# Performance work log

Hardware: AMD Instinct MI355X
Metric: run time of the kernel (lower is better)

The kernel has to match this reference:

```python
import jax, jax.numpy as jnp
import numpy as np

B, L, H, P = 4, 8192, 256, 256


def discretize(log_real, imag, log_Delta, B_real, B_imag):
    # Lambda = -exp(log_real) + i*imag ; ZOH discretization
    Lr = -jnp.exp(log_real)
    Li = imag
    Delta = jnp.exp(log_Delta)
    ad = Lr * Delta
    bd = Li * Delta
    exp_ad = jnp.exp(ad)
    Lbar_r = exp_ad * jnp.cos(bd)
    Lbar_i = exp_ad * jnp.sin(bd)
    denom = jnp.maximum(Lr * Lr + Li * Li, 1e-12)
    inv_Lr = Lr / denom
    inv_Li = -Li / denom
    diff_r = Lbar_r - 1.0
    diff_i = Lbar_i
    coeff_r = inv_Lr * diff_r - inv_Li * diff_i
    coeff_i = inv_Lr * diff_i + inv_Li * diff_r
    B_bar_r = coeff_r[:, None] * B_real - coeff_i[:, None] * B_imag
    B_bar_i = coeff_r[:, None] * B_imag + coeff_i[:, None] * B_real
    return Lbar_r, Lbar_i, B_bar_r, B_bar_i


def binop(ei, ej):
    Ar_i, Ai_i, xr_i, xi_i = ei
    Ar_j, Ai_j, xr_j, xi_j = ej
    return (Ar_j * Ar_i - Ai_j * Ai_i,
            Ar_j * Ai_i + Ai_j * Ar_i,
            Ar_j * xr_i - Ai_j * xi_i + xr_j,
            Ar_j * xi_i + Ai_j * xr_i + xi_j)


def apply_ssm(Lbar_r, Lbar_i, B_bar_r, B_bar_i, C_real, C_imag, D, x):
    # x: (B,L,H), B_bar: (P,H), C: (H,P)
    Bu_r = jnp.einsum('blh,ph->blp', x, B_bar_r)
    Bu_i = jnp.einsum('blh,ph->blp', x, B_bar_i)
    A_r = jnp.broadcast_to(Lbar_r, Bu_r.shape)
    A_i = jnp.broadcast_to(Lbar_i, Bu_i.shape)
    _, _, xs_r, xs_i = jax.lax.associative_scan(binop, (A_r, A_i, Bu_r, Bu_i), axis=1)
    ys = jnp.einsum('blp,hp->blh', xs_r, C_real) - jnp.einsum('blp,hp->blh', xs_i, C_imag)
    return ys + D * x


def s5(log_real, imag, log_Delta, B_real, B_imag, C_real, C_imag, D, x):
    Lbar_r, Lbar_i, B_bar_r, B_bar_i = discretize(log_real, imag, log_Delta, B_real, B_imag)
    y = apply_ssm(Lbar_r, Lbar_i, B_bar_r, B_bar_i, C_real, C_imag, D, x)
    return jax.nn.gelu(y, approximate=False)


def setup_inputs() -> dict:
    key = jax.random.key(0)
    ks = jax.random.split(key, 17)
    std_b = 1.0 / H ** 0.5
    std_c = 1.0 / P ** 0.5
    def params(ki):
        k = jax.random.split(ks[ki], 8)
        return dict(
            log_real=jax.random.normal(k[0], (P,), jnp.float32) * 0.5,
            imag=jax.random.normal(k[1], (P,), jnp.float32),
            log_Delta=jnp.zeros((P,), jnp.float32),
            B_real=jax.random.normal(k[2], (P, H), jnp.float32) * std_b,
            B_imag=jax.random.normal(k[3], (P, H), jnp.float32) * std_b,
            C_real=jax.random.normal(k[4], (H, P), jnp.float32) * std_c,
            C_imag=jax.random.normal(k[5], (H, P), jnp.float32) * std_c,
            D=jnp.ones((H,), jnp.float32),
        )
    f = params(1)
    b = params(2)
    inp = {'x': jax.random.normal(ks[0], (B, L, H), jnp.float32)}
    for name, v in f.items():
        inp['fwd_' + name] = v
    for name, v in b.items():
        inp['bwd_' + name] = v
    return inp


def reference(x,
              fwd_log_real, fwd_imag, fwd_log_Delta, fwd_B_real, fwd_B_imag,
              fwd_C_real, fwd_C_imag, fwd_D,
              bwd_log_real, bwd_imag, bwd_log_Delta, bwd_B_real, bwd_B_imag,
              bwd_C_real, bwd_C_imag, bwd_D):
    x_flip = jnp.flip(x, axis=1)
    y_f = s5(fwd_log_real, fwd_imag, fwd_log_Delta, fwd_B_real, fwd_B_imag,
             fwd_C_real, fwd_C_imag, fwd_D, x)
    y_b = s5(bwd_log_real, bwd_imag, bwd_log_Delta, bwd_B_real, bwd_B_imag,
             bwd_C_real, bwd_C_imag, bwd_D, x_flip)
    return y_f + jnp.flip(y_b, axis=1)
```

## Files before the change

### kernel.cpp

```cpp
#include <hip/hip_runtime.h>
#include <math.h>

#define B_DIM 4
#define L_DIM 8192
#define H_DIM 256
#define P_DIM 256
#define M_DIM (B_DIM * L_DIM)
#define NC 64
#define LC 128

typedef __attribute__((ext_vector_type(8))) short bf16x8;
typedef __attribute__((ext_vector_type(4))) float f32x4;

static __device__ __forceinline__ float bf2f(unsigned int u) {
    union { unsigned int i; float f; } v; v.i = u << 16; return v.f;
}
static __device__ __forceinline__ unsigned short f2bf(float f) {
    union { float f; unsigned int i; } v; v.f = f;
    unsigned int r = v.i + 0x7FFFu + ((v.i >> 16) & 1u);
    return (unsigned short)(r >> 16);
}
static __device__ __forceinline__ float gelu_f(float x) {
    float z = 0.7978845608028654f * (x + 0.044715f * x * x * x);
    float e = __expf(2.0f * z);
    float t = 1.0f - 2.0f / (e + 1.0f);
    return 0.5f * x * (1.0f + t);
}
static __device__ __forceinline__ void async_load16(const void* g, void* l) {
    __builtin_amdgcn_global_load_lds(
        (const __attribute__((address_space(1))) unsigned int*)g,
        (__attribute__((address_space(3))) unsigned int*)l, 16, 0, 0);
}

__global__ void prep_kernel(const float* fLr, const float* fIm, const float* fLd,
                            const float* fBr, const float* fBi,
                            const float* fCr, const float* fCi,
                            const float* bLr, const float* bIm, const float* bLd,
                            const float* bBr, const float* bBi,
                            const float* bCr, const float* bCi,
                            const float4* __restrict__ x4, ushort4* __restrict__ xb,
                            unsigned short* Bmat, unsigned short* B3, float2* LbarWS) {
    int gid = blockIdx.x * 256 + threadIdx.x;
    if (gid < 2097152) {
        float4 v = x4[gid];
        ushort4 o;
        o.x = f2bf(v.x); o.y = f2bf(v.y); o.z = f2bf(v.z); o.w = f2bf(v.w);
        xb[gid] = o;
        return;
    }
    int g1 = gid - 2097152;
    if (g1 < 262144) {
        int k = g1 >> 8, h = g1 & 255;
        int d = k >> 9, pc = k & 511, p = pc >> 1, comp = pc & 1;
        const float* LR = d ? bLr : fLr;
        const float* IM = d ? bIm : fIm;
        const float* LD = d ? bLd : fLd;
        const float* BR = d ? bBr : fBr;
        const float* BI = d ? bBi : fBi;
        float Lr = -expf(LR[p]);
        float Li = IM[p];
        float Delta = expf(LD[p]);
        float ea = expf(Lr * Delta);
        float bd = Li * Delta;
        float Lbr = ea * cosf(bd);
        float Lbi = ea * sinf(bd);
        float denom = fmaxf(Lr * Lr + Li * Li, 1e-12f);
        float ivr = Lr / denom, ivi = -Li / denom;
        float dr = Lbr - 1.0f, di = Lbi;
        float cr = ivr * dr - ivi * di;
        float ci = ivr * di + ivi * dr;
        float br = BR[p * 256 + h], bi = BI[p * 256 + h];
        float val = comp ? (cr * bi + ci * br) : (cr * br - ci * bi);
        Bmat[g1] = f2bf(val);
    } else if (g1 < 524288) {
        int g2 = g1 - 262144;
        int d = g2 >> 17;
        int rem = g2 & 131071;
        int h = rem >> 9;
        int kk = rem & 511;
        int p = kk >> 1, comp = kk & 1;
        const float* CR = d ? bCr : fCr;
        const float* CI = d ? bCi : fCi;
        float val = comp ? -CI[h * 256 + p] : CR[h * 256 + p];
        B3[g2] = f2bf(val);
    } else if (g1 < 524800) {
        int g2 = g1 - 524288;
        int d = g2 >> 8, p = g2 & 255;
        const float* LR = d ? bLr : fLr;
        const float* IM = d ? bIm : fIm;
        const float* LD = d ? bLd : fLd;
        float Lr = -expf(LR[p]); float Li = IM[p]; float Delta = expf(LD[p]);
        float ea = expf(Lr * Delta); float bd = Li * Delta;
        LbarWS[g2] = make_float2(ea * cosf(bd), ea * sinf(bd));
    }
}

__global__ __launch_bounds__(256, 2) void k1_gemm(const unsigned short* __restrict__ A,
                                                  const unsigned short* __restrict__ Bm,
                                                  unsigned short* __restrict__ Bu,
                                                  const float2* __restrict__ Lbar,
                                                  float2* __restrict__ carry,
                                                  float2* __restrict__ halfc) {
    __shared__ unsigned short SH[16384];
    __shared__ float2 Sbuf[64];
    int tid = threadIdx.x;
    int lane = tid & 63, wv = tid >> 6;
    int wm = (wv >> 1) * 64, wn = (wv & 1) * 64;
    int Mb = blockIdx.x * 128, Nb = blockIdx.y * 128;
    int lr = lane >> 3;
    int swz = ((lane & 7) ^ lr) * 8;
    f32x4 acc[4][4];
#pragma unroll
    for (int i = 0; i < 4; i++)
#pragma unroll
        for (int j = 0; j < 4; j++) acc[i][j] = (f32x4){0.f, 0.f, 0.f, 0.f};
    int mrow = lane & 15, quad = lane >> 4;
    for (int kb = 0; kb < 256; kb += 64) {
#pragma unroll
        for (int ch = wv; ch < 16; ch += 4) {
            int r = ch * 8 + lr;
            async_load16(A  + (size_t)(Mb + r) * 256 + kb + swz, (char*)SH + ch * 1024);
            async_load16(Bm + (size_t)(Nb + r) * 256 + kb + swz, (char*)SH + 16384 + ch * 1024);
        }
        __syncthreads();
#pragma unroll
        for (int kk = 0; kk < 64; kk += 32) {
            bf16x8 af[4], bfr[4];
#pragma unroll
            for (int i = 0; i < 4; i++) {
                int rr = wm + 16 * i + mrow;
                af[i] = *(const bf16x8*)&SH[rr * 64 + ((((kk >> 3) + quad) ^ (rr & 7)) << 3)];
            }
#pragma unroll
            for (int j = 0; j < 4; j++) {
                int rr = wn + 16 * j + mrow;
                bfr[j] = *(const bf16x8*)&SH[8192 + rr * 64 + ((((kk >> 3) + quad) ^ (rr & 7)) << 3)];
            }
#pragma unroll
            for (int i = 0; i < 4; i++)
#pragma unroll
                for (int j = 0; j < 4; j++)
                    acc[i][j] = __builtin_amdgcn_mfma_f32_16x16x32_bf16(af[i], bfr[j], acc[i][j], 0, 0, 0);
        }
        __syncthreads();
    }
    unsigned short* Cs = SH;
#pragma unroll
    for (int i = 0; i < 4; i++)
#pragma unroll
        for (int j = 0; j < 4; j++)
#pragma unroll
            for (int r = 0; r < 4; r++) {
                int row = wm + 16 * i + quad * 4 + r;
                int col = wn + 16 * j + mrow;
                Cs[row * 128 + col] = f2bf(acc[i][j][r]);
            }
    __syncthreads();
#pragma unroll
    for (int it = 0; it < 8; it++) {
        int o = tid * 16 + it * 4096;
        int row = o >> 8, colb = o & 255;
        uint4 v = *(const uint4*)((const char*)Cs + o);
        *(uint4*)((char*)Bu + (size_t)(Mb + row) * 2048 + (size_t)Nb * 2 + colb) = v;
    }
    int d = Nb >> 9;
    int b = Mb >> 13;
    int c = (Mb >> 7) & 63;
    float sr = 0.f, si = 0.f;
    float2 A2 = make_float2(0.f, 0.f);
    int p = 0;
    if (tid < 128) {
        int j = tid & 63, half = tid >> 6;
        p = ((Nb & 511) >> 1) + j;
        A2 = Lbar[d * 256 + p];
        const unsigned int* C32 = (const unsigned int*)Cs;
        int r0 = half * 64;
        if (d == 0) {
            for (int t = 0; t < 64; t++) {
                unsigned int v = C32[(r0 + t) * 64 + j];
                float zr = bf2f(v & 0xffffu), zi = bf2f(v >> 16);
                float nr = A2.x * sr - A2.y * si + zr;
                float ni = A2.x * si + A2.y * sr + zi;
                sr = nr; si = ni;
            }
        } else {
            for (int t = 63; t >= 0; t--) {
                unsigned int v = C32[(r0 + t) * 64 + j];
                float zr = bf2f(v & 0xffffu), zi = bf2f(v >> 16);
                float nr = A2.x * sr - A2.y * si + zr;
                float ni = A2.x * si + A2.y * sr + zi;
                sr = nr; si = ni;
            }
        }
        if (half == 1) Sbuf[j] = make_float2(sr, si);
    }
    __syncthreads();
    if (tid < 64) {
        float2 S1 = Sbuf[tid];
        float a64r = A2.x, a64i = A2.y;
#pragma unroll
        for (int k = 0; k < 6; k++) {
            float nr = a64r * a64r - a64i * a64i;
            float ni = 2.f * a64r * a64i;
            a64r = nr; a64i = ni;
        }
        float cr, ci;
        float2 hv;
        if (d == 0) {
            cr = a64r * sr - a64i * si + S1.x;
            ci = a64r * si + a64i * sr + S1.y;
            hv = make_float2(sr, si);
        } else {
            cr = sr + a64r * S1.x - a64i * S1.y;
            ci = si + a64r * S1.y + a64i * S1.x;
            hv = S1;
        }
        size_t cidx = ((size_t)(d * 4 + b) * NC + c) * 256 + p;
        carry[cidx] = make_float2(cr, ci);
        halfc[cidx] = hv;
    }
}

__global__ __launch_bounds__(512) void scan_fix_kernel(unsigned int* __restrict__ XSu,
                                                       const float2* __restrict__ Lbar,
                                                       const float2* __restrict__ carry,
                                                       const float2* __restrict__ halfc) {
    int m = blockIdx.x, b = blockIdx.y;
    int c = m >> 1, h = m & 1;
    int d = threadIdx.x >> 8;
    int p = threadIdx.x & 255;
    float2 A = Lbar[d * 256 + p];
    float ar = A.x, ai = A.y;
    float a64r = ar, a64i = ai;
#pragma unroll
    for (int k = 0; k < 6; k++) {
        float nr = a64r * a64r - a64i * a64i;
        float ni = 2.f * a64r * a64i;
        a64r = nr; a64i = ni;
    }
    float a128r = a64r * a64r - a64i * a64i;
    float a128i = 2.f * a64r * a64i;
    float sr = 0.f, si = 0.f;
    const float2* cb = carry + ((size_t)(d * 4 + b) * NC) * 256 + p;
    size_t hidx = ((size_t)(d * 4 + b) * NC + c) * 256 + p;
    if (d == 0) {
#pragma unroll 4
        for (int j = 0; j < c; j++) {
            float2 cj = cb[(size_t)j * 256];
            float nr = a128r * sr - a128i * si + cj.x;
            float ni = a128r * si + a128i * sr + cj.y;
            sr = nr; si = ni;
        }
        if (h) {
            float2 hc = halfc[hidx];
            float nr = a64r * sr - a64i * si + hc.x;
            float ni = a64r * si + a64i * sr + hc.y;
            sr = nr; si = ni;
        }
    } else {
#pragma unroll 4
        for (int j = NC - 1; j > c; j--) {
            float2 cj = cb[(size_t)j * 256];
            float nr = a128r * sr - a128i * si + cj.x;
            float ni = a128r * si + a128i * sr + cj.y;
            sr = nr; si = ni;
        }
        if (!h) {
            float2 hc = halfc[hidx];
            float nr = a64r * sr - a64i * si + hc.x;
            float ni = a64r * si + a64i * sr + hc.y;
            sr = nr; si = ni;
        }
    }
    size_t base = (size_t)b * L_DIM * 512 + d * 256 + p;
    int l0 = c * 128 + h * 64;
    if (d == 0) {
#pragma unroll 16
        for (int t = 0; t < 64; t++) {
            size_t idx = base + (size_t)(l0 + t) * 512;
            unsigned int v = XSu[idx];
            float zr = bf2f(v & 0xffffu), zi = bf2f(v >> 16);
            float nr = ar * sr - ai * si + zr;
            float ni = ar * si + ai * sr + zi;
            sr = nr; si = ni;
            XSu[idx] = (unsigned int)f2bf(sr) | ((unsigned int)f2bf(si) << 16);
        }
    } else {
#pragma unroll 16
        for (int t = 63; t >= 0; t--) {
            size_t idx = base + (size_t)(l0 + t) * 512;
            unsigned int v = XSu[idx];
            float zr = bf2f(v & 0xffffu), zi = bf2f(v >> 16);
            float nr = ar * sr - ai * si + zr;
            float ni = ar * si + ai * sr + zi;
            sr = nr; si = ni;
            XSu[idx] = (unsigned int)f2bf(sr) | ((unsigned int)f2bf(si) << 16);
        }
    }
}

static __device__ __forceinline__ void k3_half(const unsigned short* __restrict__ XS,
                                               const unsigned short* __restrict__ B3h,
                                               unsigned short* As, unsigned short* Bs,
                                               int Mb, int Hb, int coff,
                                               int wm, int wn, int mrow, int quad,
                                               int lr, int swz, int wv,
                                               f32x4 (&acc)[4][4]) {
    for (int kb = 0; kb < 512; kb += 64) {
#pragma unroll
        for (int ch = wv; ch < 16; ch += 4) {
            int r = ch * 8 + lr;
            async_load16(XS + (size_t)(Mb + r) * 1024 + coff + kb + swz, (char*)As + ch * 1024);
            async_load16(B3h + (size_t)(Hb + r) * 512 + kb + swz, (char*)Bs + ch * 1024);
        }
        __syncthreads();
#pragma unroll
        for (int kk = 0; kk < 64; kk += 32) {
            bf16x8 af[4], bfr[4];
#pragma unroll
            for (int i = 0; i < 4; i++) {
                int rr = wm + 16 * i + mrow;
                af[i] = *(const bf16x8*)&As[rr * 64 + ((((kk >> 3) + quad) ^ (rr & 7)) << 3)];
            }
#pragma unroll
            for (int j = 0; j < 4; j++) {
                int rr = wn + 16 * j + mrow;
                bfr[j] = *(const bf16x8*)&Bs[rr * 64 + ((((kk >> 3) + quad) ^ (rr & 7)) << 3)];
            }
#pragma unroll
            for (int i = 0; i < 4; i++)
#pragma unroll
                for (int j = 0; j < 4; j++)
                    acc[i][j] = __builtin_amdgcn_mfma_f32_16x16x32_bf16(af[i], bfr[j], acc[i][j], 0, 0, 0);
        }
        __syncthreads();
    }
}

__global__ __launch_bounds__(256, 2) void k3_gemm(const unsigned short* __restrict__ XS,
                                                  const unsigned short* __restrict__ B3,
                                                  const unsigned short* __restrict__ xbf,
                                                  const float* __restrict__ Df,
                                                  const float* __restrict__ Db,
                                                  float* __restrict__ out) {
    __shared__ unsigned short As[128 * 64];
    __shared__ unsigned short Bs[128 * 64];
    int tid = threadIdx.x;
    int lane = tid & 63, wv = tid >> 6;
    int wm = (wv >> 1) * 64, wn = (wv & 1) * 64;
    int Mb = blockIdx.x * 128, Hb = blockIdx.y * 128;
    int lr = lane >> 3;
    int swz = ((lane & 7) ^ lr) * 8;
    int mrow = lane & 15, quad = lane >> 4;
    f32x4 accf[4][4], accb[4][4];
#pragma unroll
    for (int i = 0; i < 4; i++)
#pragma unroll
        for (int j = 0; j < 4; j++) {
            accf[i][j] = (f32x4){0.f, 0.f, 0.f, 0.f};
            accb[i][j] = (f32x4){0.f, 0.f, 0.f, 0.f};
        }
    k3_half(XS, B3,          As, Bs, Mb, Hb, 0,   wm, wn, mrow, quad, lr, swz, wv, accf);
    k3_half(XS, B3 + 131072, As, Bs, Mb, Hb, 512, wm, wn, mrow, quad, lr, swz, wv, accb);
#pragma unroll
    for (int i = 0; i < 4; i++)
#pragma unroll
        for (int j = 0; j < 4; j++) {
            int h = Hb + wn + 16 * j + mrow;
            float df = Df[h], db = Db[h];
#pragma unroll
            for (int r = 0; r < 4; r++) {
                int row = Mb + wm + 16 * i + quad * 4 + r;
                float xv = bf2f((unsigned int)xbf[(size_t)row * 256 + h]);
                float yf = accf[i][j][r] + df * xv;
                float yb = accb[i][j][r] + db * xv;
                out[(size_t)row * 256 + h] = gelu_f(yf) + gelu_f(yb);
            }
        }
}

extern "C" void kernel_launch(void* const* d_in, const int* in_sizes, int n_in,
                              void* d_out, int out_size, void* d_ws, size_t ws_size,
                              hipStream_t stream) {
    const float* x   = (const float*)d_in[0];
    const float* fLr = (const float*)d_in[1];
    const float* fIm = (const float*)d_in[2];
    const float* fLd = (const float*)d_in[3];
    const float* fBr = (const float*)d_in[4];
    const float* fBi = (const float*)d_in[5];
    const float* fCr = (const float*)d_in[6];
    const float* fCi = (const float*)d_in[7];
    const float* fD  = (const float*)d_in[8];
    const float* bLr = (const float*)d_in[9];
    const float* bIm = (const float*)d_in[10];
    const float* bLd = (const float*)d_in[11];
    const float* bBr = (const float*)d_in[12];
    const float* bBi = (const float*)d_in[13];
    const float* bCr = (const float*)d_in[14];
    const float* bCi = (const float*)d_in[15];
    const float* bD  = (const float*)d_in[16];
    float* out = (float*)d_out;

    char* ws = (char*)d_ws;
    unsigned short* xbf  = (unsigned short*)(ws);
    unsigned short* Bu   = (unsigned short*)(ws + 16777216);
    unsigned short* Bmat = (unsigned short*)(ws + 16777216 + 67108864);
    unsigned short* B3   = (unsigned short*)(ws + 16777216 + 67108864 + 524288);
    float2* LbarWS = (float2*)(ws + 16777216 + 67108864 + 1048576);
    float2* carry  = (float2*)(ws + 16777216 + 67108864 + 1048576 + 4096);
    float2* halfc  = (float2*)(ws + 16777216 + 67108864 + 1048576 + 4096 + 1048576);

    prep_kernel<<<10242, 256, 0, stream>>>(fLr, fIm, fLd, fBr, fBi, fCr, fCi,
                                           bLr, bIm, bLd, bBr, bBi, bCr, bCi,
                                           (const float4*)x, (ushort4*)xbf,
                                           Bmat, B3, LbarWS);
    k1_gemm<<<dim3(256, 8), 256, 0, stream>>>(xbf, Bmat, Bu, LbarWS, carry, halfc);
    scan_fix_kernel<<<dim3(128, 4), 512, 0, stream>>>((unsigned int*)Bu, LbarWS, carry, halfc);
    k3_gemm<<<dim3(256, 2), 256, 0, stream>>>(Bu, B3, xbf, fD, bD, out);
}
```

Measured before the change: 198.1 us.

## Vectorize scan fixup to uint4 per thread and swap GEMM grid axes

The scan fixup kernel now has each thread handle four adjacent state channels, so it uses 16-byte loads and stores and float4 carry reads instead of 4-byte accesses. The block shrinks from 512 to 128 threads. Both GEMM kernels swap their grid x/y mapping so that blocks sharing the same M rows are launched consecutively, which should improve L2 reuse of the A operand. The trade-offs are fewer threads per block in the fixup and more serial work per thread, which lowers parallelism for a latency-bound scan.

```diff
diff --git a/kernel.cpp b/kernel.cpp
--- a/kernel.cpp
+++ b/kernel.cpp
@@ -106,7 +106,7 @@
     int tid = threadIdx.x;
     int lane = tid & 63, wv = tid >> 6;
     int wm = (wv >> 1) * 64, wn = (wv & 1) * 64;
-    int Mb = blockIdx.x * 128, Nb = blockIdx.y * 128;
+    int Mb = blockIdx.y * 128, Nb = blockIdx.x * 128;
     int lr = lane >> 3;
     int swz = ((lane & 7) ^ lr) * 8;
     f32x4 acc[4][4];
@@ -221,80 +221,115 @@
     }
 }
 
-__global__ __launch_bounds__(512) void scan_fix_kernel(unsigned int* __restrict__ XSu,
+__global__ __launch_bounds__(128) void scan_fix_kernel(uint4* __restrict__ XSu4,
                                                        const float2* __restrict__ Lbar,
                                                        const float2* __restrict__ carry,
                                                        const float2* __restrict__ halfc) {
     int m = blockIdx.x, b = blockIdx.y;
     int c = m >> 1, h = m & 1;
-    int d = threadIdx.x >> 8;
-    int p = threadIdx.x & 255;
-    float2 A = Lbar[d * 256 + p];
-    float ar = A.x, ai = A.y;
-    float a64r = ar, a64i = ai;
-#pragma unroll
-    for (int k = 0; k < 6; k++) {
-        float nr = a64r * a64r - a64i * a64i;
-        float ni = 2.f * a64r * a64i;
-        a64r = nr; a64i = ni;
-    }
-    float a128r = a64r * a64r - a64i * a64i;
-    float a128i = 2.f * a64r * a64i;
-    float sr = 0.f, si = 0.f;
-    const float2* cb = carry + ((size_t)(d * 4 + b) * NC) * 256 + p;
-    size_t hidx = ((size_t)(d * 4 + b) * NC + c) * 256 + p;
+    int d = threadIdx.x >> 6;
+    int p0 = (threadIdx.x & 63) * 4;
+    float ar[4], ai[4], a64r[4], a64i[4], a128r[4], a128i[4], sr[4], si[4];
+#pragma unroll
+    for (int j = 0; j < 4; j++) {
+        float2 A = Lbar[d * 256 + p0 + j];
+        ar[j] = A.x; ai[j] = A.y;
+        float xr = A.x, xi = A.y;
+#pragma unroll
+        for (int k = 0; k < 6; k++) {
+            float nr = xr * xr - xi * xi;
+            float ni = 2.f * xr * xi;
+            xr = nr; xi = ni;
+        }
+        a64r[j] = xr; a64i[j] = xi;
+        a128r[j] = xr * xr - xi * xi;
+        a128i[j] = 2.f * xr * xi;
+        sr[j] = 0.f; si[j] = 0.f;
+    }
+    const float4* cb4 = (const float4*)(carry + ((size_t)(d * 4 + b) * NC) * 256 + p0);
+    const float4* hb4 = (const float4*)(halfc + (((size_t)(d * 4 + b) * NC + c) * 256 + p0));
     if (d == 0) {
-#pragma unroll 4
         for (int j = 0; j < c; j++) {
-            float2 cj = cb[(size_t)j * 256];
-            float nr = a128r * sr - a128i * si + cj.x;
-            float ni = a128r * si + a128i * sr + cj.y;
-            sr = nr; si = ni;
+            float4 c01 = cb4[j * 128];
+            float4 c23 = cb4[j * 128 + 1];
+            float cx[4] = {c01.x, c01.z, c23.x, c23.z};
+            float cy[4] = {c01.y, c01.w, c23.y, c23.w};
+#pragma unroll
+            for (int q = 0; q < 4; q++) {
+                float nr = a128r[q] * sr[q] - a128i[q] * si[q] + cx[q];
+                float ni = a128r[q] * si[q] + a128i[q] * sr[q] + cy[q];
+                sr[q] = nr; si[q] = ni;
+            }
         }
         if (h) {
-            float2 hc = halfc[hidx];
-            float nr = a64r * sr - a64i * si + hc.x;
-            float ni = a64r * si + a64i * sr + hc.y;
-            sr = nr; si = ni;
+            float4 h01 = hb4[0], h23 = hb4[1];
+            float hx[4] = {h01.x, h01.z, h23.x, h23.z};
+            float hy[4] = {h01.y, h01.w, h23.y, h23.w};
+#pragma unroll
+            for (int q = 0; q < 4; q++) {
+                float nr = a64r[q] * sr[q] - a64i[q] * si[q] + hx[q];
+                float ni = a64r[q] * si[q] + a64i[q] * sr[q] + hy[q];
+                sr[q] = nr; si[q] = ni;
+            }
         }
     } else {
-#pragma unroll 4
         for (int j = NC - 1; j > c; j--) {
-            float2 cj = cb[(size_t)j * 256];
-            float nr = a128r * sr - a128i * si + cj.x;
-            float ni = a128r * si + a128i * sr + cj.y;
-            sr = nr; si = ni;
+            float4 c01 = cb4[j * 128];
+            float4 c23 = cb4[j * 128 + 1];
+            float cx[4] = {c01.x, c01.z, c23.x, c23.z};
+            float cy[4] = {c01.y, c01.w, c23.y, c23.w};
+#pragma unroll
+            for (int q = 0; q < 4; q++) {
+                float nr = a128r[q] * sr[q] - a128i[q] * si[q] + cx[q];
+                float ni = a128r[q] * si[q] + a128i[q] * sr[q] + cy[q];
+                sr[q] = nr; si[q] = ni;
+            }
         }
         if (!h) {
-            float2 hc = halfc[hidx];
-            float nr = a64r * sr - a64i * si + hc.x;
-            float ni = a64r * si + a64i * sr + hc.y;
-            sr = nr; si = ni;
-        }
-    }
-    size_t base = (size_t)b * L_DIM * 512 + d * 256 + p;
+            float4 h01 = hb4[0], h23 = hb4[1];
+            float hx[4] = {h01.x, h01.z, h23.x, h23.z};
+            float hy[4] = {h01.y, h01.w, h23.y, h23.w};
+#pragma unroll
+            for (int q = 0; q < 4; q++) {
+                float nr = a64r[q] * sr[q] - a64i[q] * si[q] + hx[q];
+                float ni = a64r[q] * si[q] + a64i[q] * sr[q] + hy[q];
+                sr[q] = nr; si[q] = ni;
+            }
+        }
+    }
+    size_t base = (size_t)b * L_DIM * 128 + d * 64 + (p0 >> 2);
     int l0 = c * 128 + h * 64;
     if (d == 0) {
-#pragma unroll 16
+#pragma unroll 8
         for (int t = 0; t < 64; t++) {
-            size_t idx = base + (size_t)(l0 + t) * 512;
-            unsigned int v = XSu[idx];
-            float zr = bf2f(v & 0xffffu), zi = bf2f(v >> 16);
-            float nr = ar * sr - ai * si + zr;
-            float ni = ar * si + ai * sr + zi;
-            sr = nr; si = ni;
-            XSu[idx] = (unsigned int)f2bf(sr) | ((unsigned int)f2bf(si) << 16);
+            size_t idx = base + (size_t)(l0 + t) * 128;
+            uint4 v = XSu4[idx];
+            unsigned int u[4] = {v.x, v.y, v.z, v.w};
+#pragma unroll
+            for (int q = 0; q < 4; q++) {
+                float zr = bf2f(u[q] & 0xffffu), zi = bf2f(u[q] >> 16);
+                float nr = ar[q] * sr[q] - ai[q] * si[q] + zr;
+                float ni = ar[q] * si[q] + ai[q] * sr[q] + zi;
+                sr[q] = nr; si[q] = ni;
+                u[q] = (unsigned int)f2bf(sr[q]) | ((unsigned int)f2bf(si[q]) << 16);
+            }
+            XSu4[idx] = make_uint4(u[0], u[1], u[2], u[3]);
         }
     } else {
-#pragma unroll 16
+#pragma unroll 8
         for (int t = 63; t >= 0; t--) {
-            size_t idx = base + (size_t)(l0 + t) * 512;
-            unsigned int v = XSu[idx];
-            float zr = bf2f(v & 0xffffu), zi = bf2f(v >> 16);
-            float nr = ar * sr - ai * si + zr;
-            float ni = ar * si + ai * sr + zi;
-            sr = nr; si = ni;
-            XSu[idx] = (unsigned int)f2bf(sr) | ((unsigned int)f2bf(si) << 16);
+            size_t idx = base + (size_t)(l0 + t) * 128;
+            uint4 v = XSu4[idx];
+            unsigned int u[4] = {v.x, v.y, v.z, v.w};
+#pragma unroll
+            for (int q = 0; q < 4; q++) {
+                float zr = bf2f(u[q] & 0xffffu), zi = bf2f(u[q] >> 16);
+                float nr = ar[q] * sr[q] - ai[q] * si[q] + zr;
+                float ni = ar[q] * si[q] + ai[q] * sr[q] + zi;
+                sr[q] = nr; si[q] = ni;
+                u[q] = (unsigned int)f2bf(sr[q]) | ((unsigned int)f2bf(si[q]) << 16);
+            }
+            XSu4[idx] = make_uint4(u[0], u[1], u[2], u[3]);
         }
     }
 }
@@ -348,7 +383,7 @@
     int tid = threadIdx.x;
     int lane = tid & 63, wv = tid >> 6;
     int wm = (wv >> 1) * 64, wn = (wv & 1) * 64;
-    int Mb = blockIdx.x * 128, Hb = blockIdx.y * 128;
+    int Mb = blockIdx.y * 128, Hb = blockIdx.x * 128;
     int lr = lane >> 3;
     int swz = ((lane & 7) ^ lr) * 8;
     int mrow = lane & 15, quad = lane >> 4;
@@ -414,7 +449,7 @@
                                            bLr, bIm, bLd, bBr, bBi, bCr, bCi,
                                            (const float4*)x, (ushort4*)xbf,
                                            Bmat, B3, LbarWS);
-    k1_gemm<<<dim3(256, 8), 256, 0, stream>>>(xbf, Bmat, Bu, LbarWS, carry, halfc);
-    scan_fix_kernel<<<dim3(128, 4), 512, 0, stream>>>((unsigned int*)Bu, LbarWS, carry, halfc);
-    k3_gemm<<<dim3(256, 2), 256, 0, stream>>>(Bu, B3, xbf, fD, bD, out);
-}
+    k1_gemm<<<dim3(8, 256), 256, 0, stream>>>(xbf, Bmat, Bu, LbarWS, carry, halfc);
+    scan_fix_kernel<<<dim3(128, 4), 128, 0, stream>>>((uint4*)Bu, LbarWS, carry, halfc);
+    k3_gemm<<<dim3(2, 256), 256, 0, stream>>>(Bu, B3, xbf, fD, bD, out);
+}
```

Result: slower. 216.8 us (+9.4%).
